# Optimization experiments

Measured on AMD Instinct MI355X. Metric: run time of the kernel, lower is better.

The kernel has to match this reference:

```python
import jax, jax.numpy as jnp
import numpy as np
from jax import lax

V, E, H, S = 50000, 512, 512, 16384


def setup_inputs() -> dict:
    key = jax.random.key(0)
    ks = jax.random.split(key, 10)
    sc_e = 1.0 / np.sqrt(E)
    sc_h = 1.0 / np.sqrt(H)
    return {
        "x": jax.random.randint(ks[0], (S,), 0, V, dtype=jnp.int64)
        if jax.config.jax_enable_x64
        else jax.random.randint(ks[0], (S,), 0, V, dtype=jnp.int32),
        "emb_table": jax.random.normal(ks[1], (V, E), dtype=jnp.float32),
        "W_ih": jax.random.uniform(ks[2], (4 * H, E), jnp.float32, -sc_h, sc_h),
        "W_hh": jax.random.uniform(ks[3], (4 * H, H), jnp.float32, -sc_h, sc_h),
        "b_ih": jax.random.uniform(ks[4], (4 * H,), jnp.float32, -sc_h, sc_h),
        "b_hh": jax.random.uniform(ks[5], (4 * H,), jnp.float32, -sc_h, sc_h),
        "W1": jax.random.uniform(ks[6], (128, H), jnp.float32, -sc_h, sc_h),
        "b1": jax.random.uniform(ks[7], (128,), jnp.float32, -sc_h, sc_h),
        "W2": jax.random.uniform(ks[8], (9, 128), jnp.float32, -1 / np.sqrt(128), 1 / np.sqrt(128)),
        "b2": jax.random.uniform(ks[9], (9,), jnp.float32, -1 / np.sqrt(128), 1 / np.sqrt(128)),
    }


def reference(x, emb_table, W_ih, W_hh, b_ih, b_hh, W1, b1, W2, b2):
    # Embedding lookup: [S, E]  (batch=1 via view(1,-1,E) in the original)
    w2v = emb_table[x]
    # Precompute input contributions to the 4 gates for all timesteps: [S, 4H]
    gx = w2v @ W_ih.T + (b_ih + b_hh)

    def step(carry, gxt):
        h, c = carry
        g = gxt + h @ W_hh.T  # [4H]; torch gate order: i, f, g, o
        i = jax.nn.sigmoid(g[:H])
        f = jax.nn.sigmoid(g[H : 2 * H])
        gg = jnp.tanh(g[2 * H : 3 * H])
        o = jax.nn.sigmoid(g[3 * H :])
        c = f * c + i * gg
        h = o * jnp.tanh(c)
        return (h, c), None

    h0 = jnp.zeros((H,), dtype=w2v.dtype)
    c0 = jnp.zeros((H,), dtype=w2v.dtype)
    (h_last, _), _ = lax.scan(step, (h0, c0), gx)

    out = jax.nn.sigmoid(h_last @ W1.T + b1)
    out = jax.nn.sigmoid(out @ W2.T + b2)
    return out[None, :]  # [1, 9], matching out[:, -1, :] batch dim
```

## Files before the change

kernel.cpp:

```cpp
#include <hip/hip_runtime.h>
#include <hip/hip_bf16.h>


#define S_LEN 16384
#define NWG   16
#define NLAUNCH 256
#define NTHR  512

typedef unsigned long long u64;
typedef float float4v __attribute__((ext_vector_type(4)));

static __device__ __forceinline__ float bf2f(unsigned int u16) {
  union { unsigned int i; float f; } v; v.i = u16 << 16; return v.f;
}
static __device__ __forceinline__ unsigned short f2bf(float f) {
  union { float f; unsigned int i; } v; v.f = f;
  unsigned int r = v.i + 0x7fffu + ((v.i >> 16) & 1u);
  return (unsigned short)(r >> 16);
}
static __device__ __forceinline__ float fsig(float x) { return 1.f / (1.f + __expf(-x)); }
static __device__ __forceinline__ float ftanh(float x) { return 2.f / (1.f + __expf(-2.f * x)) - 1.f; }

static __device__ __forceinline__ int haddr(int k) { return k + (k >> 4); }

__global__ __launch_bounds__(256, 2) void gx_gemm(
    const int* __restrict__ x, const float* __restrict__ emb,
    const float* __restrict__ W_ih, const float* __restrict__ b_ih,
    const float* __restrict__ b_hh, unsigned short* __restrict__ gx)
{
  __shared__ float As[64][40];
  __shared__ float Bs[64][40];
  __shared__ int   xs[64];

  const int tid = threadIdx.x;
  const int bm = blockIdx.x;
  const int bn = blockIdx.y;

  if (tid < 64) xs[tid] = x[bm * 64 + tid];
  __syncthreads();

  float acc[4][4] = {};
  const int r0 = (tid >> 4) * 4;
  const int c0 = tid & 15;

  for (int kc = 0; kc < 512; kc += 32) {
#pragma unroll
    for (int h = 0; h < 2; ++h) {
      const int v = tid + h * 256;
      const int row = v >> 3, k4 = v & 7;
      const float4 av = *(const float4*)(emb + (size_t)xs[row] * 512 + kc + k4 * 4);
      As[row][k4 * 4 + 0] = av.x; As[row][k4 * 4 + 1] = av.y;
      As[row][k4 * 4 + 2] = av.z; As[row][k4 * 4 + 3] = av.w;
      const float4 bv = *(const float4*)(W_ih + (size_t)(bn * 64 + row) * 512 + kc + k4 * 4);
      Bs[row][k4 * 4 + 0] = bv.x; Bs[row][k4 * 4 + 1] = bv.y;
      Bs[row][k4 * 4 + 2] = bv.z; Bs[row][k4 * 4 + 3] = bv.w;
    }
    __syncthreads();
#pragma unroll
    for (int k4 = 0; k4 < 8; ++k4) {
      float4 a[4], b[4];
#pragma unroll
      for (int i = 0; i < 4; ++i) a[i] = *(const float4*)&As[r0 + i][k4 * 4];
#pragma unroll
      for (int j = 0; j < 4; ++j) b[j] = *(const float4*)&Bs[c0 + j * 16][k4 * 4];
#pragma unroll
      for (int i = 0; i < 4; ++i)
#pragma unroll
        for (int j = 0; j < 4; ++j) {
          acc[i][j] = __builtin_fmaf(a[i].x, b[j].x, acc[i][j]);
          acc[i][j] = __builtin_fmaf(a[i].y, b[j].y, acc[i][j]);
          acc[i][j] = __builtin_fmaf(a[i].z, b[j].z, acc[i][j]);
          acc[i][j] = __builtin_fmaf(a[i].w, b[j].w, acc[i][j]);
        }
    }
    __syncthreads();
  }

#pragma unroll
  for (int j = 0; j < 4; ++j) {
    const int c = bn * 64 + c0 + j * 16;
    const float bias = b_ih[c] + b_hh[c];
    const size_t dstc = (size_t)(c & 511) * 4 + (size_t)(c >> 9);
#pragma unroll
    for (int i = 0; i < 4; ++i) {
      const size_t t = (size_t)bm * 64 + r0 + i;
      gx[t * 2048 + dstc] = f2bf(acc[i][j] + bias);
    }
  }
}

__global__ __launch_bounds__(NTHR, 1) void lstm_rec(
    const float* __restrict__ W_hh, const unsigned short* __restrict__ gx,
    const float* __restrict__ W1, const float* __restrict__ b1,
    const float* __restrict__ W2, const float* __restrict__ b2,
    float* __restrict__ out,
    unsigned int* __restrict__ h32,
    unsigned int* __restrict__ done)
{
  const int tid = threadIdx.x;
  const int w   = blockIdx.x;

  if (w >= NWG) {
    float a0 = (float)tid, a1 = a0 + 1.f, a2 = a0 + 2.f, a3 = a0 + 3.f;
    for (;;) {
      if (__hip_atomic_load(done, __ATOMIC_RELAXED, __HIP_MEMORY_SCOPE_AGENT))
        break;
#pragma unroll 32
      for (int i = 0; i < 512; ++i) {
        a0 = __builtin_fmaf(a0, 1.0000001f, 1e-9f);
        a1 = __builtin_fmaf(a1, 0.9999999f, 1e-9f);
        a2 = __builtin_fmaf(a2, 1.0000002f, 1e-9f);
        a3 = __builtin_fmaf(a3, 0.9999998f, 1e-9f);
      }
    }
    asm volatile("" :: "v"(a0), "v"(a1), "v"(a2), "v"(a3));
    return;
  }

  const int s    = tid & 31;
  const int half = (tid >> 5) & 1;
  const int wvi  = tid >> 6;
  const int ubase  = w * 32 + wvi * 4 + half * 2;
  const int ulocal = wvi * 4 + half * 2;

  float4v wvv[32];
#pragma unroll
  for (int q = 0; q < 8; ++q) {
    const int row = (q & 3) * 512 + ubase + (q >> 2);
    const float* src = W_hh + (size_t)row * 512 + s * 16;
#pragma unroll
    for (int i4 = 0; i4 < 4; ++i4) {
      asm volatile("global_load_dwordx4 %0, %1, off\n\ts_waitcnt vmcnt(0)"
                   : "=v"(wvv[q * 4 + i4]) : "v"((u64)(src + i4 * 4)) : "memory");
    }
  }

  __shared__ float hbuf[2][544];

  float c0 = 0.f, c1 = 0.f;
  float h_reg[16];
#pragma unroll
  for (int i = 0; i < 16; ++i) h_reg[i] = 0.f;

  uint4 g_cur = {0,0,0,0}, g_nxt = {0,0,0,0};
  if (s == 0) {
    g_cur = *(const uint4*)(gx + (size_t)0 * 2048 + ubase * 4);
    g_nxt = *(const uint4*)(gx + (size_t)1 * 2048 + ubase * 4);
  }

  for (int t = 0; t < S_LEN; ++t) {
    uint4 g_new = {0,0,0,0};
    if (s == 0 && t + 2 < S_LEN)
      g_new = *(const uint4*)(gx + (size_t)(t + 2) * 2048 + ubase * 4);

    float acc[8];
#pragma unroll
    for (int q = 0; q < 8; ++q) {
      float a = 0.f;
#pragma unroll
      for (int i4 = 0; i4 < 4; ++i4) {
        const float4v vv = wvv[q * 4 + i4];
        a = __builtin_fmaf(vv.x, h_reg[i4 * 4 + 0], a);
        a = __builtin_fmaf(vv.y, h_reg[i4 * 4 + 1], a);
        a = __builtin_fmaf(vv.z, h_reg[i4 * 4 + 2], a);
        a = __builtin_fmaf(vv.w, h_reg[i4 * 4 + 3], a);
      }
      acc[q] = a;
    }
#pragma unroll
    for (int q = 0; q < 8; ++q) {
      float a = acc[q];
      a += __shfl_xor(a, 1);
      a += __shfl_xor(a, 2);
      a += __shfl_xor(a, 4);
      a += __shfl_xor(a, 8);
      a += __shfl_xor(a, 16);
      acc[q] = a;
    }

    const int buf = (t + 1) & 1;
    if (s == 0) {
      const float pi0 = acc[0] + bf2f(g_cur.x & 0xffffu);
      const float pf0 = acc[1] + bf2f(g_cur.x >> 16);
      const float pg0 = acc[2] + bf2f(g_cur.y & 0xffffu);
      const float po0 = acc[3] + bf2f(g_cur.y >> 16);
      const float pi1 = acc[4] + bf2f(g_cur.z & 0xffffu);
      const float pf1 = acc[5] + bf2f(g_cur.z >> 16);
      const float pg1 = acc[6] + bf2f(g_cur.w & 0xffffu);
      const float po1 = acc[7] + bf2f(g_cur.w >> 16);
      c0 = fsig(pf0) * c0 + fsig(pi0) * ftanh(pg0);
      c1 = fsig(pf1) * c1 + fsig(pi1) * ftanh(pg1);
      const float h0 = fsig(po0) * ftanh(c0);
      const float h1 = fsig(po1) * ftanh(c1);
      const unsigned tg16 = (unsigned)(t + 1) << 16;
      const unsigned w0 = tg16 | (unsigned)f2bf(h0);
      const unsigned w1 = tg16 | (unsigned)f2bf(h1);
      const u64 pk = ((u64)w1 << 32) | (u64)w0;
      __hip_atomic_store((u64*)&h32[buf * 512 + w * 32 + ulocal], pk,
                         __ATOMIC_RELAXED, __HIP_MEMORY_SCOPE_AGENT);
    }

    if (tid < 64 && t + 1 < S_LEN) {
      const u64* hb = (const u64*)(h32 + buf * 512);
      const unsigned want = (unsigned)(t + 1) & 0xffffu;
      u64 v[4];
      for (;;) {
#pragma unroll
        for (int j = 0; j < 4; ++j)
          v[j] = __hip_atomic_load(&hb[j * 64 + tid],
                                   __ATOMIC_RELAXED, __HIP_MEMORY_SCOPE_AGENT);
        bool ok = true;
#pragma unroll
        for (int j = 0; j < 4; ++j) {
          ok &= (((unsigned)(v[j] >> 16) & 0xffffu) == want);
          ok &= ((unsigned)(v[j] >> 48) == want);
        }
        if (__all(ok)) break;
      }
#pragma unroll
      for (int j = 0; j < 4; ++j) {
        const int k = (j * 64 + tid) * 2;
        const unsigned lo = (unsigned)v[j];
        const unsigned hi = (unsigned)(v[j] >> 32);
        union { unsigned u; float f; } f0, f1;
        f0.u = lo << 16; f1.u = hi << 16;
        hbuf[buf][haddr(k)]     = f0.f;
        hbuf[buf][haddr(k + 1)] = f1.f;
      }
    }
    __syncthreads();

    if (t + 1 < S_LEN) {
      const int base = s * 17;
#pragma unroll
      for (int i = 0; i < 16; ++i)
        h_reg[i] = hbuf[buf][base + i];
    }

    g_cur = g_nxt; g_nxt = g_new;
  }

  if (w == 0 && tid == 0)
    __hip_atomic_store(done, 1u, __ATOMIC_RELAXED, __HIP_MEMORY_SCOPE_AGENT);

  if (w == 0) {
    __shared__ float hl[512];
    __shared__ float zl[128];
    {
      unsigned v;
      do {
        v = __hip_atomic_load(&h32[tid], __ATOMIC_RELAXED, __HIP_MEMORY_SCOPE_AGENT);
      } while ((v >> 16) != (unsigned)S_LEN);
      union { unsigned u; float f; } hu; hu.u = v << 16;
      hl[tid] = hu.f;
    }
    __syncthreads();
    const int j = tid >> 2, q = tid & 3;
    float sum = 0.f;
    const float4* w1v = (const float4*)(W1 + (size_t)j * 512 + q * 128);
#pragma unroll 8
    for (int k4 = 0; k4 < 32; ++k4) {
      const float4 v = w1v[k4];
      const int kb = q * 128 + k4 * 4;
      sum = __builtin_fmaf(v.x, hl[kb + 0], sum);
      sum = __builtin_fmaf(v.y, hl[kb + 1], sum);
      sum = __builtin_fmaf(v.z, hl[kb + 2], sum);
      sum = __builtin_fmaf(v.w, hl[kb + 3], sum);
    }
    sum += __shfl_xor(sum, 1);
    sum += __shfl_xor(sum, 2);
    if (q == 0) zl[j] = fsig(sum + b1[j]);
    __syncthreads();
    if (tid < 9) {
      float o = b2[tid];
      const float* w2r = W2 + tid * 128;
#pragma unroll 16
      for (int k = 0; k < 128; ++k) o = __builtin_fmaf(w2r[k], zl[k], o);
      out[tid] = fsig(o);
    }
  }
}

extern "C" void kernel_launch(void* const* d_in, const int* in_sizes, int n_in,
                              void* d_out, int out_size, void* d_ws, size_t ws_size,
                              hipStream_t stream) {
  const int*   x     = (const int*)d_in[0];
  const float* emb   = (const float*)d_in[1];
  const float* W_ih  = (const float*)d_in[2];
  const float* W_hh  = (const float*)d_in[3];
  const float* b_ih  = (const float*)d_in[4];
  const float* b_hh  = (const float*)d_in[5];
  const float* W1    = (const float*)d_in[6];
  const float* b1    = (const float*)d_in[7];
  const float* W2    = (const float*)d_in[8];
  const float* b2    = (const float*)d_in[9];
  float* out = (float*)d_out;

  const size_t gx_bytes = (size_t)S_LEN * 2048 * sizeof(unsigned short);
  const size_t h_off    = gx_bytes;
  const size_t dn_off   = h_off + 8192;
  if (ws_size < h_off + 16384) return;

  unsigned short* gxp  = (unsigned short*)d_ws;
  unsigned int*   h32  = (unsigned int*)((char*)d_ws + h_off);
  unsigned int*   done = (unsigned int*)((char*)d_ws + dn_off);

  (void)hipMemsetAsync((char*)d_ws + h_off, 0, 16384, stream);

  dim3 g1(S_LEN / 64, 2048 / 64);
  gx_gemm<<<g1, 256, 0, stream>>>(x, emb, W_ih, b_ih, b_hh, gxp);
  lstm_rec<<<NLAUNCH, NTHR, 0, stream>>>(W_hh, gxp, W1, b1, W2, b2, out,
                                         h32, done);
}
```

Baseline: 47.94 ms.

## Stage h values in LDS and publish with one coalesced store per block

Each block now gathers its new hidden values in shared memory after a barrier, then one wave writes all 16 packed pairs to global memory together, instead of 16 scattered per-wave atomic stores. The stored values are unchanged; the goal is less memory traffic on the latency-critical step-to-step handoff. The 240 idle busy-spin blocks now each poll their own padded done flag and poll four times less often, which cuts contention on the flag cache line. The trade-off is an extra __syncthreads per timestep before the publish, which can lengthen the recurrence's critical path.

```diff
diff --git a/kernel.cpp b/kernel.cpp
--- a/kernel.cpp
+++ b/kernel.cpp
@@ -101,12 +101,13 @@
   const int w   = blockIdx.x;
 
   if (w >= NWG) {
+    unsigned int* myflag = done + (w - NWG) * 8;
     float a0 = (float)tid, a1 = a0 + 1.f, a2 = a0 + 2.f, a3 = a0 + 3.f;
     for (;;) {
-      if (__hip_atomic_load(done, __ATOMIC_RELAXED, __HIP_MEMORY_SCOPE_AGENT))
+      if (__hip_atomic_load(myflag, __ATOMIC_RELAXED, __HIP_MEMORY_SCOPE_AGENT))
         break;
 #pragma unroll 32
-      for (int i = 0; i < 512; ++i) {
+      for (int i = 0; i < 2048; ++i) {
         a0 = __builtin_fmaf(a0, 1.0000001f, 1e-9f);
         a1 = __builtin_fmaf(a1, 0.9999999f, 1e-9f);
         a2 = __builtin_fmaf(a2, 1.0000002f, 1e-9f);
@@ -136,6 +137,7 @@
   }
 
   __shared__ float hbuf[2][544];
+  __shared__ unsigned int stage[32];
 
   float c0 = 0.f, c1 = 0.f;
   float h_reg[16];
@@ -193,39 +195,44 @@
       const float h0 = fsig(po0) * ftanh(c0);
       const float h1 = fsig(po1) * ftanh(c1);
       const unsigned tg16 = (unsigned)(t + 1) << 16;
-      const unsigned w0 = tg16 | (unsigned)f2bf(h0);
-      const unsigned w1 = tg16 | (unsigned)f2bf(h1);
-      const u64 pk = ((u64)w1 << 32) | (u64)w0;
-      __hip_atomic_store((u64*)&h32[buf * 512 + w * 32 + ulocal], pk,
-                         __ATOMIC_RELAXED, __HIP_MEMORY_SCOPE_AGENT);
-    }
-
-    if (tid < 64 && t + 1 < S_LEN) {
-      const u64* hb = (const u64*)(h32 + buf * 512);
-      const unsigned want = (unsigned)(t + 1) & 0xffffu;
-      u64 v[4];
-      for (;;) {
-#pragma unroll
-        for (int j = 0; j < 4; ++j)
-          v[j] = __hip_atomic_load(&hb[j * 64 + tid],
-                                   __ATOMIC_RELAXED, __HIP_MEMORY_SCOPE_AGENT);
-        bool ok = true;
+      const u64 pk = ((u64)(tg16 | (unsigned)f2bf(h1)) << 32)
+                   |  (u64)(tg16 | (unsigned)f2bf(h0));
+      *(u64*)&stage[ulocal] = pk;
+    }
+    __syncthreads();
+
+    if (tid < 64) {
+      if (tid < 16) {
+        const u64 sv = *(const u64*)&stage[tid * 2];
+        __hip_atomic_store((u64*)&h32[buf * 512 + w * 32] + tid, sv,
+                           __ATOMIC_RELAXED, __HIP_MEMORY_SCOPE_AGENT);
+      }
+      if (t + 1 < S_LEN) {
+        const u64* hb = (const u64*)(h32 + buf * 512);
+        const unsigned want = (unsigned)(t + 1) & 0xffffu;
+        u64 v[4];
+        for (;;) {
+#pragma unroll
+          for (int j = 0; j < 4; ++j)
+            v[j] = __hip_atomic_load(&hb[j * 64 + tid],
+                                     __ATOMIC_RELAXED, __HIP_MEMORY_SCOPE_AGENT);
+          bool ok = true;
+#pragma unroll
+          for (int j = 0; j < 4; ++j) {
+            ok &= (((unsigned)(v[j] >> 16) & 0xffffu) == want);
+            ok &= ((unsigned)(v[j] >> 48) == want);
+          }
+          if (__all(ok)) break;
+        }
 #pragma unroll
         for (int j = 0; j < 4; ++j) {
-          ok &= (((unsigned)(v[j] >> 16) & 0xffffu) == want);
-          ok &= ((unsigned)(v[j] >> 48) == want);
+          const int k = (j * 64 + tid) * 2;
+          union { unsigned u; float f; } f0, f1;
+          f0.u = ((unsigned)v[j]) << 16;
+          f1.u = ((unsigned)(v[j] >> 32)) << 16;
+          hbuf[buf][haddr(k)]     = f0.f;
+          hbuf[buf][haddr(k + 1)] = f1.f;
         }
-        if (__all(ok)) break;
-      }
-#pragma unroll
-      for (int j = 0; j < 4; ++j) {
-        const int k = (j * 64 + tid) * 2;
-        const unsigned lo = (unsigned)v[j];
-        const unsigned hi = (unsigned)(v[j] >> 32);
-        union { unsigned u; float f; } f0, f1;
-        f0.u = lo << 16; f1.u = hi << 16;
-        hbuf[buf][haddr(k)]     = f0.f;
-        hbuf[buf][haddr(k + 1)] = f1.f;
       }
     }
     __syncthreads();
@@ -240,8 +247,9 @@
     g_cur = g_nxt; g_nxt = g_new;
   }
 
-  if (w == 0 && tid == 0)
-    __hip_atomic_store(done, 1u, __ATOMIC_RELAXED, __HIP_MEMORY_SCOPE_AGENT);
+  if (w == 0 && tid < NLAUNCH - NWG)
+    __hip_atomic_store(done + tid * 8, 1u,
+                       __ATOMIC_RELAXED, __HIP_MEMORY_SCOPE_AGENT);
 
   if (w == 0) {
     __shared__ float hl[512];
@@ -298,7 +306,7 @@
 
   const size_t gx_bytes = (size_t)S_LEN * 2048 * sizeof(unsigned short);
   const size_t h_off    = gx_bytes;
-  const size_t dn_off   = h_off + 8192;
+  const size_t dn_off   = h_off + 4096;
   if (ws_size < h_off + 16384) return;
 
   unsigned short* gxp  = (unsigned short*)d_ws;
```

After: 45.48 ms. 5.1% less time.
